# Performance work log

Measured on AMD Instinct MI355X. Metric: run time of the kernel, lower is better.

## Reference

```python
import jax, jax.numpy as jnp
import numpy as np

B, L, D_MODEL = 2, 2048, 1024
EXPAND, D_STATE, D_CONV = 2, 16, 4
D_INNER = EXPAND * D_MODEL          # 2048
DT_RANK = D_MODEL // 16             # 64 (mamba-ssm 'auto' rank)


def setup_inputs() -> dict:
    key = jax.random.key(0)
    ks = jax.random.split(key, 8)
    s = lambda k, shape, scale: jax.random.normal(k, shape, jnp.float32) * scale
    x = s(ks[0], (B, L, D_MODEL), 1.0)
    W_in = s(ks[1], (2 * D_INNER, D_MODEL), D_MODEL ** -0.5)
    conv_w = s(ks[2], (D_INNER, 1, D_CONV), D_CONV ** -0.5)   # depthwise kernel
    conv_b = s(ks[3], (D_INNER,), 0.02)
    W_xproj = s(ks[4], (DT_RANK + 2 * D_STATE, D_INNER), D_INNER ** -0.5)
    W_dt = s(ks[5], (D_INNER, DT_RANK), DT_RANK ** -0.5)
    # inverse-softplus of dt ~= 0.01 (mamba default dt init region)
    b_dt = jnp.log(jnp.expm1(0.01 * jnp.ones((D_INNER,), jnp.float32)))
    # S4D-real init: A = -[1..d_state] per channel
    A_log = jnp.log(jnp.broadcast_to(
        jnp.arange(1, D_STATE + 1, dtype=jnp.float32), (D_INNER, D_STATE)))
    D = jnp.ones((D_INNER,), jnp.float32)
    W_out = s(ks[6], (D_MODEL, D_INNER), D_INNER ** -0.5)
    return dict(x=x, W_in=W_in, conv_w=conv_w, conv_b=conv_b, W_xproj=W_xproj,
                W_dt=W_dt, b_dt=b_dt, A_log=A_log, D=D, W_out=W_out)


def reference(x, W_in, conv_w, conv_b, W_xproj, W_dt, b_dt, A_log, D, W_out):
    # in_proj: [B,L,d_model] -> [B,L,2*d_inner]
    xz = jnp.einsum('bld,ed->ble', x, W_in)
    xs, z = jnp.split(xz, 2, axis=-1)

    # causal depthwise conv1d over time, kernel d_conv
    xc = jnp.swapaxes(xs, 1, 2)  # [B, d_inner, L]
    xc = jax.lax.conv_general_dilated(
        xc, conv_w, window_strides=(1,), padding=[(D_CONV - 1, 0)],
        feature_group_count=D_INNER)
    xc = xc + conv_b[None, :, None]
    xs = jax.nn.silu(jnp.swapaxes(xc, 1, 2))  # [B,L,d_inner]

    # x_proj -> (dt, B, C)
    x_dbl = jnp.einsum('bld,ed->ble', xs, W_xproj)
    dt, Bm, Cm = jnp.split(x_dbl, [DT_RANK, DT_RANK + D_STATE], axis=-1)
    dt = jax.nn.softplus(jnp.einsum('blr,dr->bld', dt, W_dt) + b_dt)  # [B,L,d_inner]

    A = -jnp.exp(A_log)  # [d_inner, d_state]

    def step(h, inp):
        dt_t, B_t, C_t, x_t = inp  # [B,d], [B,n], [B,n], [B,d]
        dA = jnp.exp(dt_t[..., None] * A)                       # [B,d,n]
        h = h * dA + (dt_t * x_t)[..., None] * B_t[:, None, :]  # [B,d,n]
        y = jnp.einsum('bdn,bn->bd', h, C_t)
        return h, y

    tm = lambda a: jnp.swapaxes(a, 0, 1)  # time-major for scan
    h0 = jnp.zeros((x.shape[0], D_INNER, D_STATE), x.dtype)
    _, ys = jax.lax.scan(step, h0, (tm(dt), tm(Bm), tm(Cm), tm(xs)))

    y = tm(ys) + xs * D          # skip term D*x
    y = y * jax.nn.silu(z)       # gate
    return jnp.einsum('bld,ed->ble', y, W_out)  # out_proj -> [B,L,d_model]
```

## Files before the change

kernel.cpp:

```cpp
#include <hip/hip_runtime.h>
#include <cstdint>
#include <cstddef>

typedef __bf16 bf16_t;
typedef bf16_t bf16x4 __attribute__((ext_vector_type(4)));
typedef bf16_t bf16x8 __attribute__((ext_vector_type(8)));
typedef float f32x4 __attribute__((ext_vector_type(4)));

static __device__ __forceinline__ void glds16(const void* g, void* l) {
    __builtin_amdgcn_global_load_lds((const __attribute__((address_space(1))) void*)g,
                                     (__attribute__((address_space(3))) void*)l,
                                     16, 0, 0);
}

#define BARRIER()  asm volatile("s_barrier" ::: "memory")
#define DS_WAIT()  do { asm volatile("s_waitcnt lgkmcnt(0)" ::: "memory"); \
                        __builtin_amdgcn_sched_barrier(0); } while (0)

__global__ __launch_bounds__(256)
void cast5(const float* __restrict__ s0, bf16_t* __restrict__ d0, int n0,
           const float* __restrict__ s1, bf16_t* __restrict__ d1, int n1,
           const float* __restrict__ s2, bf16_t* __restrict__ d2, int n2,
           const float* __restrict__ s3, bf16_t* __restrict__ d3, int n3,
           const float* __restrict__ s4, bf16_t* __restrict__ d4)
{
    int bb = blockIdx.x;
    const float* s; bf16_t* d;
    if (bb < n0)              { s = s0; d = d0; }
    else if ((bb -= n0) < n1) { s = s1; d = d1; }
    else if ((bb -= n1) < n2) { s = s2; d = d2; }
    else if ((bb -= n2) < n3) { s = s3; d = d3; }
    else                      { bb -= n3; s = s4; d = d4; }
    const size_t base = (size_t)bb * 1024 + threadIdx.x * 4;
    const f32x4 v = *(const f32x4*)(s + base);
    bf16x4 o;
    o[0] = (bf16_t)v[0]; o[1] = (bf16_t)v[1]; o[2] = (bf16_t)v[2]; o[3] = (bf16_t)v[3];
    *(bf16x4*)(d + base) = o;
}

#define LOAD_A(MQ) \
    _Pragma("unroll") for (int mf = 0; mf < 4; ++mf) { \
        aF[mf][0] = *(const bf16x8*)(Ab + (aRow + (MQ)*64 + mf*16)*64 + ck0); \
        aF[mf][1] = *(const bf16x8*)(Ab + (aRow + (MQ)*64 + mf*16)*64 + ck1); }

#define LOAD_B(NQ, dst) \
    _Pragma("unroll") for (int nf = 0; nf < 2; ++nf) { \
        dst[nf][0] = *(const bf16x8*)(Bb + (bRow + (NQ)*32 + nf*16)*64 + ck0); \
        dst[nf][1] = *(const bf16x8*)(Bb + (bRow + (NQ)*32 + nf*16)*64 + ck1); }

#define MFMA16(MQ, NQ, bset) \
    __builtin_amdgcn_s_setprio(1); \
    _Pragma("unroll") for (int mf = 0; mf < 4; ++mf) \
    _Pragma("unroll") for (int nf = 0; nf < 2; ++nf) \
    _Pragma("unroll") for (int kk = 0; kk < 2; ++kk) \
        acc[(MQ)*4+mf][(NQ)*2+nf] = __builtin_amdgcn_mfma_f32_16x16x32_bf16( \
            aF[mf][kk], bset[nf][kk], acc[(MQ)*4+mf][(NQ)*2+nf], 0, 0, 0); \
    __builtin_amdgcn_s_setprio(0);

template<int EPI, int SPLITK>
__global__ __launch_bounds__(512, 2)
void gemm256_bt(const bf16_t* __restrict__ A, const bf16_t* __restrict__ Bt,
                const int N, const int K, const int KC,
                bf16_t* __restrict__ o0, bf16_t* __restrict__ o1)
{
    constexpr int TILE = 256 * 64;
    __shared__ __align__(16) bf16_t As[2 * TILE];
    __shared__ __align__(16) bf16_t Bs[2 * TILE];

    const int tid  = threadIdx.x;
    const int lane = tid & 63;
    const int w    = tid >> 6;
    const int wm   = w >> 2, wn = w & 3;
    const int l16  = lane & 15, quad = lane >> 4;
    const int e7   = l16 & 7;
    const int ck0  = (quad ^ e7) << 3;
    const int ck1  = ck0 ^ 32;
    const int lr   = lane >> 3, l8 = lane & 7;
    const int swz  = (l8 ^ lr) << 3;
    const int m0   = blockIdx.y * 256, n0 = blockIdx.x * 256;
    const int NT   = KC >> 6;

    const int aRow = wm * 128 + l16;
    const int bRow = wn * 64 + l16;

    f32x4 acc[8][4] = {};
    bf16x8 aF[4][2], bLo[2][2], bHi[2][2];

    auto STAGE = [&](int unit, int kt, int d) {
        const bf16_t* g; int rg0; bf16_t* lb; int rbase;
        if (unit <= 1) { g = A;  rg0 = m0; lb = As;
                         rbase = unit * 64 + w * 8; }
        else           { g = Bt; rg0 = n0; lb = Bs;
                         rbase = ((w >> 2) << 6) + ((w & 3) << 3) + ((unit & 1) << 5); }
#pragma unroll
        for (int L = 0; L < 2; ++L) {
            const int rb = rbase + L * 128;
            glds16(g + (size_t)(rg0 + rb + lr) * K + kt * 64 + swz,
                   lb + d * TILE + rb * 64);
        }
    };

    STAGE(2, 0, 0); STAGE(0, 0, 0); STAGE(3, 0, 0); STAGE(1, 0, 0);
    if (NT > 1) { STAGE(2, 1, 1); STAGE(0, 1, 1); STAGE(3, 1, 1); }
    if (NT > 1) asm volatile("s_waitcnt vmcnt(6)" ::: "memory");
    else        asm volatile("s_waitcnt vmcnt(0)" ::: "memory");
    BARRIER();

    for (int i = 0; i < NT; ++i) {
        const int b = i & 1;
        const bf16_t* Ab = As + b * TILE;
        const bf16_t* Bb = Bs + b * TILE;

        LOAD_A(0); LOAD_B(0, bLo);
        if (i + 1 < NT) STAGE(1, i + 1, (i + 1) & 1);
        BARRIER(); DS_WAIT();
        MFMA16(0, 0, bLo);
        __builtin_amdgcn_sched_barrier(0);
        BARRIER();

        LOAD_B(1, bHi);
        if (i + 2 < NT) STAGE(2, i + 2, b);
        BARRIER(); DS_WAIT();
        MFMA16(0, 1, bHi);
        __builtin_amdgcn_sched_barrier(0);
        BARRIER();

        LOAD_A(1);
        if (i + 2 < NT) { STAGE(0, i + 2, b); STAGE(3, i + 2, b); }
        BARRIER(); DS_WAIT();
        MFMA16(1, 1, bHi);
        MFMA16(1, 0, bLo);
        __builtin_amdgcn_sched_barrier(0);
        if (i + 2 < NT) asm volatile("s_waitcnt vmcnt(6)" ::: "memory");
        else            asm volatile("s_waitcnt vmcnt(0)" ::: "memory");
        BARRIER();
    }

#pragma unroll
    for (int mf = 0; mf < 8; ++mf)
#pragma unroll
        for (int nf = 0; nf < 4; ++nf)
#pragma unroll
            for (int r = 0; r < 4; ++r) {
                const int gr = m0 + wm * 128 + mf * 16 + quad * 4 + r;
                const int gc = n0 + wn * 64 + nf * 16 + l16;
                const float v = acc[mf][nf][r];
                if (EPI == 1) {
                    if (gc < 2048) o0[(size_t)gr * 2048 + gc] = (bf16_t)v;
                    else           o1[(size_t)gr * 2048 + (gc - 2048)] = (bf16_t)v;
                } else {
                    ((float*)o0)[(size_t)gr * N + gc] = v;
                }
            }
}

template<int EPI>
__global__ __launch_bounds__(256)
void gemm_bt(const bf16_t* __restrict__ A, const bf16_t* __restrict__ Bt,
             const int M, const int N, const int K,
             void* __restrict__ o0, void* __restrict__ o1,
             const float* __restrict__ bias)
{
    __shared__ __align__(16) bf16_t As[128 * 64];
    __shared__ __align__(16) bf16_t Bs[128 * 64];

    const int tid  = threadIdx.x;
    const int lane = tid & 63;
    const int wave = tid >> 6;
    const int wm = wave & 1, wn = wave >> 1;
    const int m0 = blockIdx.y * 128, n0 = blockIdx.x * 128;
    const int quad = lane >> 4, l16 = lane & 15;

    f32x4 acc[4][4] = {};

    for (int k0 = 0; k0 < K; k0 += 64) {
        __syncthreads();
#pragma unroll
        for (int j = 0; j < 4; j++) {
            const int u  = wave * 2048 + j * 512;
            const int ue = u + lane * 8;
            const int row = ue >> 6, col = ue & 63;
            glds16(A  + (size_t)(m0 + row) * K + k0 + col, As + u);
            glds16(Bt + (size_t)(n0 + row) * K + k0 + col, Bs + u);
        }
        __syncthreads();

#pragma unroll
        for (int kk = 0; kk < 2; kk++) {
            bf16x8 afr[4], bfr[4];
#pragma unroll
            for (int mt = 0; mt < 4; mt++)
                afr[mt] = *(const bf16x8*)(As + (wm * 64 + mt * 16 + l16) * 64 + kk * 32 + quad * 8);
#pragma unroll
            for (int nt = 0; nt < 4; nt++)
                bfr[nt] = *(const bf16x8*)(Bs + (wn * 64 + nt * 16 + l16) * 64 + kk * 32 + quad * 8);
#pragma unroll
            for (int mt = 0; mt < 4; mt++)
#pragma unroll
                for (int nt = 0; nt < 4; nt++)
                    acc[mt][nt] = __builtin_amdgcn_mfma_f32_16x16x32_bf16(
                        afr[mt], bfr[nt], acc[mt][nt], 0, 0, 0);
        }
    }

#pragma unroll
    for (int mt = 0; mt < 4; mt++)
#pragma unroll
        for (int nt = 0; nt < 4; nt++)
#pragma unroll
            for (int r = 0; r < 4; r++) {
                const int gr = m0 + wm * 64 + mt * 16 + quad * 4 + r;
                const int gc = n0 + wn * 64 + nt * 16 + l16;
                const float v = acc[mt][nt][r];
                if (EPI == 0) {
                    ((float*)o0)[(size_t)gr * N + gc] = v;
                } else if (EPI == 2) {
                    const float t  = v + bias[gc];
                    const float sp = (t > 15.f) ? t : __logf(1.f + __expf(t));
                    ((bf16_t*)o0)[(size_t)gr * 2048 + gc] = (bf16_t)sp;
                }
            }
}

__global__ __launch_bounds__(256)
void conv_xproj_dt(const bf16_t* __restrict__ xs_pre,
                   const float* __restrict__ cw, const float* __restrict__ cb,
                   const bf16_t* __restrict__ Wxp, const bf16_t* __restrict__ Wdt,
                   const float* __restrict__ bdt,
                   bf16_t* __restrict__ xs, bf16_t* __restrict__ dt,
                   float* __restrict__ Bm, float* __restrict__ Cm)
{
    __shared__ __align__(16) bf16_t xsL[16 * 2048];
    __shared__ float red[4][64][25];
    __shared__ __align__(16) bf16_t dtA[16 * 64];

    const int tid  = threadIdx.x;
    const int lane = tid & 63, w = tid >> 6;
    const int m0   = blockIdx.x * 16;
    const int l16  = lane & 15, quad = lane >> 4, l8 = lane & 7;
    const int l0   = m0 & 2047;

    {
        const int d0 = tid * 8;
        float w0[8], w1[8], w2[8], w3[8], bs[8];
#pragma unroll
        for (int j = 0; j < 8; j++) {
            const f32x4 wv = *(const f32x4*)(cw + (size_t)(d0 + j) * 4);
            w0[j] = wv[0]; w1[j] = wv[1]; w2[j] = wv[2]; w3[j] = wv[3];
            bs[j] = cb[d0 + j];
        }
        const int r1 = (m0 >= 1) ? m0 - 1 : 0;
        const int r2 = (m0 >= 2) ? m0 - 2 : 0;
        const int r3 = (m0 >= 3) ? m0 - 3 : 0;
        const bf16x8 v1 = *(const bf16x8*)(xs_pre + (size_t)r1 * 2048 + d0);
        const bf16x8 v2 = *(const bf16x8*)(xs_pre + (size_t)r2 * 2048 + d0);
        const bf16x8 v3 = *(const bf16x8*)(xs_pre + (size_t)r3 * 2048 + d0);
        float p1[8], p2[8], p3[8];
#pragma unroll
        for (int j = 0; j < 8; j++) {
            p1[j] = (float)v1[j]; p2[j] = (float)v2[j]; p3[j] = (float)v3[j];
        }
#pragma unroll
        for (int r = 0; r < 16; r++) {
            const int l = l0 + r;
            const float m1 = (l >= 1) ? 1.f : 0.f;
            const float m2 = (l >= 2) ? 1.f : 0.f;
            const float m3 = (l >= 3) ? 1.f : 0.f;
            const bf16x8 v = *(const bf16x8*)(xs_pre + (size_t)(m0 + r) * 2048 + d0);
            bf16x8 o;
#pragma unroll
            for (int j = 0; j < 8; j++) {
                const float cur = (float)v[j];
                float a = bs[j] + w3[j] * cur;
                a += m1 * w2[j] * p1[j];
                a += m2 * w1[j] * p2[j];
                a += m3 * w0[j] * p3[j];
                const float s = a / (1.f + __expf(-a));
                o[j] = (bf16_t)s;
                p3[j] = p2[j]; p2[j] = p1[j]; p1[j] = cur;
            }
            *(bf16x8*)(xs + (size_t)(m0 + r) * 2048 + d0) = o;
            const int g = (d0 >> 3) ^ (r & 7);
            *(bf16x8*)(xsL + r * 2048 + g * 8) = o;
        }
    }
    __syncthreads();

    f32x4 acc[6] = {};
    const int kbase = w * 512;
    for (int k0 = 0; k0 < 512; k0 += 32) {
        const int gA = ((kbase + k0) >> 3) + quad;
        const bf16x8 afr = *(const bf16x8*)(xsL + (size_t)l16 * 2048 + ((gA ^ l8) << 3));
#pragma unroll
        for (int t = 0; t < 6; t++) {
            const bf16x8 bfr = *(const bf16x8*)(Wxp + (size_t)(t * 16 + l16) * 2048 + kbase + k0 + quad * 8);
            acc[t] = __builtin_amdgcn_mfma_f32_16x16x32_bf16(afr, bfr, acc[t], 0, 0, 0);
        }
    }
#pragma unroll
    for (int t = 0; t < 6; t++)
#pragma unroll
        for (int r = 0; r < 4; r++) red[w][lane][t * 4 + r] = acc[t][r];
    __syncthreads();

    {
#pragma unroll
        for (int r = 0; r < 4; r++) {
            const int j = w * 4 + r;
            const float v = red[0][lane][j] + red[1][lane][j]
                          + red[2][lane][j] + red[3][lane][j];
            const int row = quad * 4 + r, col = w * 16 + l16;
            const int g = (col >> 3) ^ (row & 7);
            dtA[row * 64 + g * 8 + (col & 7)] = (bf16_t)v;
        }
        if (w == 0) {
#pragma unroll
            for (int t = 4; t < 6; t++)
#pragma unroll
                for (int r = 0; r < 4; r++) {
                    const int j = t * 4 + r;
                    const float v = red[0][lane][j] + red[1][lane][j]
                                  + red[2][lane][j] + red[3][lane][j];
                    const int gr = m0 + quad * 4 + r;
                    const int gc = t * 16 + l16;
                    if (gc < 80) Bm[(size_t)gr * 16 + (gc - 64)] = v;
                    else         Cm[(size_t)gr * 16 + (gc - 80)] = v;
                }
        }
    }
    __syncthreads();

    const bf16x8 a0 = *(const bf16x8*)(dtA + l16 * 64 + (((0 + quad) ^ l8) << 3));
    const bf16x8 a1 = *(const bf16x8*)(dtA + l16 * 64 + (((4 + quad) ^ l8) << 3));
    for (int nt = 0; nt < 32; ++nt) {
        const int nb = w * 512 + nt * 16;
        const bf16x8 b0 = *(const bf16x8*)(Wdt + (size_t)(nb + l16) * 64 + quad * 8);
        const bf16x8 b1 = *(const bf16x8*)(Wdt + (size_t)(nb + l16) * 64 + 32 + quad * 8);
        f32x4 a = {};
        a = __builtin_amdgcn_mfma_f32_16x16x32_bf16(a0, b0, a, 0, 0, 0);
        a = __builtin_amdgcn_mfma_f32_16x16x32_bf16(a1, b1, a, 0, 0, 0);
        const int gc = nb + l16;
        const float bv = bdt[gc];
#pragma unroll
        for (int r = 0; r < 4; r++) {
            const int gr = m0 + quad * 4 + r;
            const float t  = a[r] + bv;
            const float sp = (t > 15.f) ? t : __logf(1.f + __expf(t));
            dt[(size_t)gr * 2048 + gc] = (bf16_t)sp;
        }
    }
}

__global__ __launch_bounds__(256)
void conv_silu(const bf16_t* __restrict__ xs_pre, const float* __restrict__ cw,
               const float* __restrict__ cb, bf16_t* __restrict__ xs)
{
    const int d0 = threadIdx.x * 8;
    const int rg = blockIdx.x * 8;
    float w0[8], w1[8], w2[8], w3[8], bs[8];
#pragma unroll
    for (int j = 0; j < 8; j++) {
        const f32x4 wv = *(const f32x4*)(cw + (size_t)(d0 + j) * 4);
        w0[j] = wv[0]; w1[j] = wv[1]; w2[j] = wv[2]; w3[j] = wv[3];
        bs[j] = cb[d0 + j];
    }
    float p1[8], p2[8], p3[8];
    {
        const int r1 = (rg >= 1) ? rg - 1 : 0;
        const int r2 = (rg >= 2) ? rg - 2 : 0;
        const int r3 = (rg >= 3) ? rg - 3 : 0;
        const bf16x8 v1 = *(const bf16x8*)(xs_pre + (size_t)r1 * 2048 + d0);
        const bf16x8 v2 = *(const bf16x8*)(xs_pre + (size_t)r2 * 2048 + d0);
        const bf16x8 v3 = *(const bf16x8*)(xs_pre + (size_t)r3 * 2048 + d0);
#pragma unroll
        for (int j = 0; j < 8; j++) {
            p1[j] = (float)v1[j]; p2[j] = (float)v2[j]; p3[j] = (float)v3[j];
        }
    }
#pragma unroll
    for (int t = 0; t < 8; t++) {
        const int r = rg + t;
        const int l = r & 2047;
        const float m1 = (l >= 1) ? 1.f : 0.f;
        const float m2 = (l >= 2) ? 1.f : 0.f;
        const float m3 = (l >= 3) ? 1.f : 0.f;
        const bf16x8 v = *(const bf16x8*)(xs_pre + (size_t)r * 2048 + d0);
        bf16x8 o;
#pragma unroll
        for (int j = 0; j < 8; j++) {
            const float cur = (float)v[j];
            float a = bs[j] + w3[j] * cur;
            a += m1 * w2[j] * p1[j];
            a += m2 * w1[j] * p2[j];
            a += m3 * w0[j] * p3[j];
            const float s = a / (1.f + __expf(-a));
            o[j] = (bf16_t)s;
            p3[j] = p2[j]; p2[j] = p1[j]; p1[j] = cur;
        }
        *(bf16x8*)(xs + (size_t)r * 2048 + d0) = o;
    }
}

__global__ __launch_bounds__(256)
void xproj_kernel(const bf16_t* __restrict__ A, const bf16_t* __restrict__ Bt,
                  bf16_t* __restrict__ dtr, float* __restrict__ Bm, float* __restrict__ Cm)
{
    __shared__ float red[4][64][25];
    const int tid  = threadIdx.x;
    const int lane = tid & 63, w = tid >> 6;
    const int m0 = blockIdx.x * 16;
    const int l16 = lane & 15, quad = lane >> 4;
    f32x4 acc[6] = {};

    const int kbase = w * 512;
    const bf16_t* ap = A + (size_t)(m0 + l16) * 2048 + kbase + quad * 8;
    for (int k0 = 0; k0 < 512; k0 += 32) {
        const bf16x8 afr = *(const bf16x8*)(ap + k0);
#pragma unroll
        for (int t = 0; t < 6; t++) {
            const bf16x8 bfr = *(const bf16x8*)(Bt + (size_t)(t * 16 + l16) * 2048 + kbase + k0 + quad * 8);
            acc[t] = __builtin_amdgcn_mfma_f32_16x16x32_bf16(afr, bfr, acc[t], 0, 0, 0);
        }
    }
#pragma unroll
    for (int t = 0; t < 6; t++)
#pragma unroll
        for (int r = 0; r < 4; r++) red[w][lane][t * 4 + r] = acc[t][r];
    __syncthreads();
    if (w == 0) {
#pragma unroll
        for (int t = 0; t < 6; t++)
#pragma unroll
            for (int r = 0; r < 4; r++) {
                const int j = t * 4 + r;
                const float v = red[0][lane][j] + red[1][lane][j]
                              + red[2][lane][j] + red[3][lane][j];
                const int gr = m0 + quad * 4 + r;
                const int gc = t * 16 + l16;
                if (gc < 64)      dtr[(size_t)gr * 64 + gc] = (bf16_t)v;
                else if (gc < 80) Bm[(size_t)gr * 16 + (gc - 64)] = v;
                else              Cm[(size_t)gr * 16 + (gc - 80)] = v;
            }
    }
}

static __device__ __forceinline__ bool fast_check(const float* A_log, int d, float& a1) {
    a1 = -__expf(A_log[(size_t)d * 16]);
    bool ok = true;
#pragma unroll
    for (int n = 1; n < 16; n++) {
        const float an = -__expf(A_log[(size_t)d * 16 + n]);
        const float pn = (float)(n + 1) * a1;
        ok = ok && (fabsf(an - pn) <= 1e-3f * fabsf(pn) + 1e-6f);
    }
    return ok;
}

__global__ __launch_bounds__(256)
void scan1(const bf16_t* __restrict__ dt, const bf16_t* __restrict__ xs,
           const float* __restrict__ Bm, const float* __restrict__ A_log,
           float* __restrict__ sdt_o, bf16_t* __restrict__ Hsum)
{
    const int tid = threadIdx.x;
    const int bi  = blockIdx.x;
    const int c   = bi & 63;
    const int bb  = bi >> 6;
    const int b   = bb >> 3;
    const int d   = (bb & 7) * 256 + tid;
    float a1; const bool fast = fast_check(A_log, d, a1);

    float h[16] = {};
    float s = 0.f;
    const size_t rowbase = (size_t)b * 2048 + c * 32;

    if (fast) {
#pragma unroll 4
        for (int t = 0; t < 32; t++) {
            const size_t ro = (rowbase + t) * 2048 + d;
            const float dtv = (float)dt[ro];
            const float xv  = (float)xs[ro];
            s += dtv;
            const float r = __expf(dtv * a1);
            float rp[16]; rp[0] = r;
#pragma unroll
            for (int n = 1; n < 16; n++) rp[n] = rp[n - 1] * r;
            const float bx = dtv * xv;
            const float* bp = Bm + (rowbase + t) * 16;
#pragma unroll
            for (int n = 0; n < 16; n++) h[n] = fmaf(h[n], rp[n], bx * bp[n]);
        }
    } else {
        for (int t = 0; t < 32; t++) {
            const size_t ro = (rowbase + t) * 2048 + d;
            const float dtv = (float)dt[ro];
            const float xv  = (float)xs[ro];
            s += dtv;
            const float bx = dtv * xv;
            const float* bp = Bm + (rowbase + t) * 16;
#pragma unroll
            for (int n = 0; n < 16; n++) {
                const float an = -__expf(A_log[(size_t)d * 16 + n]);
                h[n] = fmaf(h[n], __expf(dtv * an), bx * bp[n]);
            }
        }
    }
    const size_t sb = (size_t)bi * 256 + tid;
    sdt_o[sb] = s;
    bf16x8 h0, h1;
#pragma unroll
    for (int n = 0; n < 8; n++) { h0[n] = (bf16_t)h[n]; h1[n] = (bf16_t)h[n + 8]; }
    *(bf16x8*)(Hsum + sb * 16)     = h0;
    *(bf16x8*)(Hsum + sb * 16 + 8) = h1;
}

__global__ __launch_bounds__(256)
void scan2(const float* __restrict__ sdt, bf16_t* __restrict__ Hsum,
           const float* __restrict__ A_log)
{
    const int tid = threadIdx.x;
    const int bb  = blockIdx.x;
    const int d   = (bb & 7) * 256 + tid;
    float a1; const bool fast = fast_check(A_log, d, a1);

    float h[16] = {};
    if (fast) {
        size_t sb = (size_t)(bb * 64) * 256 + tid;
        float sA = sdt[sb];
        bf16x8 hA0 = *(const bf16x8*)(Hsum + sb * 16);
        bf16x8 hA1 = *(const bf16x8*)(Hsum + sb * 16 + 8);
        float sB = 0.f; bf16x8 hB0 = {}, hB1 = {};
        {
            const size_t sb1 = sb + 256;
            sB  = sdt[sb1];
            hB0 = *(const bf16x8*)(Hsum + sb1 * 16);
            hB1 = *(const bf16x8*)(Hsum + sb1 * 16 + 8);
        }
        for (int c = 0; c < 64; c++) {
            float sC = 0.f; bf16x8 hC0 = {}, hC1 = {};
            if (c + 2 < 64) {
                const size_t sb2 = sb + 512;
                sC  = sdt[sb2];
                hC0 = *(const bf16x8*)(Hsum + sb2 * 16);
                hC1 = *(const bf16x8*)(Hsum + sb2 * 16 + 8);
            }
            bf16x8 o0, o1;
#pragma unroll
            for (int n = 0; n < 8; n++) { o0[n] = (bf16_t)h[n]; o1[n] = (bf16_t)h[n + 8]; }
            *(bf16x8*)(Hsum + sb * 16)     = o0;
            *(bf16x8*)(Hsum + sb * 16 + 8) = o1;
            const float r = __expf(sA * a1);
            float rp[16]; rp[0] = r;
#pragma unroll
            for (int n = 1; n < 16; n++) rp[n] = rp[n - 1] * r;
#pragma unroll
            for (int n = 0; n < 16; n++) {
                const float hsv = (n < 8) ? (float)hA0[n] : (float)hA1[n - 8];
                h[n] = fmaf(h[n], rp[n], hsv);
            }
            sb += 256;
            sA = sB; hA0 = hB0; hA1 = hB1;
            sB = sC; hB0 = hC0; hB1 = hC1;
        }
    } else {
        for (int c = 0; c < 64; c++) {
            const size_t sb = ((size_t)(bb * 64 + c) * 256 + tid);
            const float s = sdt[sb];
            bf16x8 hs0 = *(const bf16x8*)(Hsum + sb * 16);
            bf16x8 hs1 = *(const bf16x8*)(Hsum + sb * 16 + 8);
            bf16x8 o0, o1;
#pragma unroll
            for (int n = 0; n < 8; n++) { o0[n] = (bf16_t)h[n]; o1[n] = (bf16_t)h[n + 8]; }
            *(bf16x8*)(Hsum + sb * 16)     = o0;
            *(bf16x8*)(Hsum + sb * 16 + 8) = o1;
#pragma unroll
            for (int n = 0; n < 16; n++) {
                const float an = -__expf(A_log[(size_t)d * 16 + n]);
                const float hsv = (n < 8) ? (float)hs0[n] : (float)hs1[n - 8];
                h[n] = fmaf(h[n], __expf(s * an), hsv);
            }
        }
    }
}

__global__ __launch_bounds__(256)
void scan3(const bf16_t* __restrict__ dt, const bf16_t* __restrict__ xs,
           bf16_t* __restrict__ zy,
           const float* __restrict__ Bm, const float* __restrict__ Cm,
           const float* __restrict__ A_log, const float* __restrict__ Dv,
           const bf16_t* __restrict__ Hseed)
{
    const int tid = threadIdx.x;
    const int bi  = blockIdx.x;
    const int c   = bi & 63;
    const int bb  = bi >> 6;
    const int b   = bb >> 3;
    const int d   = (bb & 7) * 256 + tid;
    float a1; const bool fast = fast_check(A_log, d, a1);
    const float Dd = Dv[d];

    const size_t sb = (size_t)bi * 256 + tid;
    const bf16x8 hs0 = *(const bf16x8*)(Hseed + sb * 16);
    const bf16x8 hs1 = *(const bf16x8*)(Hseed + sb * 16 + 8);
    float h[16];
#pragma unroll
    for (int n = 0; n < 8; n++) { h[n] = (float)hs0[n]; h[n + 8] = (float)hs1[n]; }

    const size_t rowbase = (size_t)b * 2048 + c * 32;

    if (fast) {
#pragma unroll 2
        for (int t = 0; t < 32; t++) {
            const size_t ro = (rowbase + t) * 2048 + d;
            const float dtv = (float)dt[ro];
            const float xv  = (float)xs[ro];
            const float zv  = (float)zy[ro];
            const float r = __expf(dtv * a1);
            float rp[16]; rp[0] = r;
#pragma unroll
            for (int n = 1; n < 16; n++) rp[n] = rp[n - 1] * r;
            const float bx = dtv * xv;
            const float* bp = Bm + (rowbase + t) * 16;
            const float* cp = Cm + (rowbase + t) * 16;
            float y0 = 0.f, y1 = 0.f;
#pragma unroll
            for (int n = 0; n < 16; n += 2) {
                h[n]     = fmaf(h[n],     rp[n],     bx * bp[n]);
                h[n + 1] = fmaf(h[n + 1], rp[n + 1], bx * bp[n + 1]);
                y0 = fmaf(h[n],     cp[n],     y0);
                y1 = fmaf(h[n + 1], cp[n + 1], y1);
            }
            const float yv = (y0 + y1) + xv * Dd;
            const float g  = zv / (1.f + __expf(-zv));
            zy[ro] = (bf16_t)(yv * g);
        }
    } else {
        for (int t = 0; t < 32; t++) {
            const size_t ro = (rowbase + t) * 2048 + d;
            const float dtv = (float)dt[ro];
            const float xv  = (float)xs[ro];
            const float zv  = (float)zy[ro];
            const float bx = dtv * xv;
            const float* bp = Bm + (rowbase + t) * 16;
            const float* cp = Cm + (rowbase + t) * 16;
            float y = 0.f;
#pragma unroll
            for (int n = 0; n < 16; n++) {
                const float an = -__expf(A_log[(size_t)d * 16 + n]);
                h[n] = fmaf(h[n], __expf(dtv * an), bx * bp[n]);
                y = fmaf(h[n], cp[n], y);
            }
            const float yv = y + xv * Dd;
            const float g  = zv / (1.f + __expf(-zv));
            zy[ro] = (bf16_t)(yv * g);
        }
    }
}

extern "C" void kernel_launch(void* const* d_in, const int* in_sizes, int n_in,
                              void* d_out, int out_size, void* d_ws, size_t ws_size,
                              hipStream_t stream)
{
    const float* x     = (const float*)d_in[0];
    const float* W_in  = (const float*)d_in[1];
    const float* convw = (const float*)d_in[2];
    const float* convb = (const float*)d_in[3];
    const float* W_xp  = (const float*)d_in[4];
    const float* W_dt  = (const float*)d_in[5];
    const float* b_dt  = (const float*)d_in[6];
    const float* A_log = (const float*)d_in[7];
    const float* Dv    = (const float*)d_in[8];
    const float* W_out = (const float*)d_in[9];

    char* ws = (char*)d_ws;
    bf16_t* bufP   = (bf16_t*)(ws + 0);
    bf16_t* bufZ   = (bf16_t*)(ws + 16777216);
    bf16_t* bufX   = (bf16_t*)(ws + 33554432);
    bf16_t* W_in_b = (bf16_t*)(ws + 33554432);
    bf16_t* dtr    = (bf16_t*)(ws + 50331648);
    float*  Bm     = (float*)(ws + 50855936);
    float*  Cm     = (float*)(ws + 51118080);
    float*  sdt    = (float*)(ws + 51380224);
    bf16_t* Hsum   = (bf16_t*)(ws + 52428800);
    bf16_t* x_b    = (bf16_t*)(ws + 52428800);
    bf16_t* W_out_b= (bf16_t*)(ws + 60817408);
    bf16_t* W_xp_b = (bf16_t*)(ws + 65011712);
    bf16_t* W_dt_b = (bf16_t*)(ws + 65404928);
    bf16_t* dtb    = (bf16_t*)(ws + 65667072);
    const bool fuse = (ws_size >= 82444288ull);

    cast5<<<dim3(4096 + 4096 + 2048 + 192 + 128), dim3(256), 0, stream>>>(
        x, x_b, 4096, W_in, W_in_b, 4096, W_out, W_out_b, 2048,
        W_xp, W_xp_b, 192, W_dt, W_dt_b);

    gemm256_bt<1, 1><<<dim3(16, 16), dim3(512), 0, stream>>>(
        x_b, W_in_b, 4096, 1024, 1024, bufP, bufZ);

    bf16_t* dtp = fuse ? dtb : bufP;
    if (fuse) {
        conv_xproj_dt<<<dim3(256), dim3(256), 0, stream>>>(
            bufP, convw, convb, W_xp_b, W_dt_b, b_dt, bufX, dtb, Bm, Cm);
    } else {
        conv_silu<<<dim3(512), dim3(256), 0, stream>>>(bufP, convw, convb, bufX);
        xproj_kernel<<<dim3(256), dim3(256), 0, stream>>>(bufX, W_xp_b, dtr, Bm, Cm);
        gemm_bt<2><<<dim3(16, 32), dim3(256), 0, stream>>>(
            dtr, W_dt_b, 4096, 2048, 64, (void*)bufP, nullptr, b_dt);
    }

    scan1<<<dim3(1024), dim3(256), 0, stream>>>(dtp, bufX, Bm, A_log, sdt, Hsum);
    scan2<<<dim3(16),   dim3(256), 0, stream>>>(sdt, Hsum, A_log);
    scan3<<<dim3(1024), dim3(256), 0, stream>>>(dtp, bufX, bufZ, Bm, Cm, A_log, Dv, Hsum);

    gemm_bt<0><<<dim3(8, 32), dim3(256), 0, stream>>>(
        bufZ, W_out_b, 4096, 1024, 2048, d_out, nullptr, nullptr);
}
```

Measured before the change: 280.8 us.

## Store xs and dt channel-major for scans; split-K the output projection

The conv and dt-projection kernels now write xs and dt transposed as [d_inner, B*L], so each scan thread can read its 32 time steps as contiguous bf16x8 vectors instead of one scalar per step with a 2048-element stride. The output GEMM is split along K into two halves that accumulate with atomic adds into an output zeroed by a memset, which doubles the block count. The costs are an extra memset, atomic traffic, and strided scalar loads in the non-fused xproj path. The z gate in scan3 is still read row-major.

```diff
diff --git a/kernel.cpp b/kernel.cpp
--- a/kernel.cpp
+++ b/kernel.cpp
@@ -154,7 +154,7 @@
             }
 }
 
-template<int EPI>
+template<int EPI, int SPLITK>
 __global__ __launch_bounds__(256)
 void gemm_bt(const bf16_t* __restrict__ A, const bf16_t* __restrict__ Bt,
              const int M, const int N, const int K,
@@ -170,10 +170,13 @@
     const int wm = wave & 1, wn = wave >> 1;
     const int m0 = blockIdx.y * 128, n0 = blockIdx.x * 128;
     const int quad = lane >> 4, l16 = lane & 15;
+    const int z   = (SPLITK > 1) ? blockIdx.z : 0;
+    const int KC  = K / SPLITK;
+    const int kb  = z * KC;
 
     f32x4 acc[4][4] = {};
 
-    for (int k0 = 0; k0 < K; k0 += 64) {
+    for (int k0 = kb; k0 < kb + KC; k0 += 64) {
         __syncthreads();
 #pragma unroll
         for (int j = 0; j < 4; j++) {
@@ -212,12 +215,14 @@
                 const int gr = m0 + wm * 64 + mt * 16 + quad * 4 + r;
                 const int gc = n0 + wn * 64 + nt * 16 + l16;
                 const float v = acc[mt][nt][r];
-                if (EPI == 0) {
-                    ((float*)o0)[(size_t)gr * N + gc] = v;
+                if (EPI == 4) {
+                    unsafeAtomicAdd((float*)o0 + (size_t)gr * N + gc, v);
                 } else if (EPI == 2) {
                     const float t  = v + bias[gc];
                     const float sp = (t > 15.f) ? t : __logf(1.f + __expf(t));
-                    ((bf16_t*)o0)[(size_t)gr * 2048 + gc] = (bf16_t)sp;
+                    ((bf16_t*)o0)[(size_t)gc * 4096 + gr] = (bf16_t)sp;
+                } else {
+                    ((float*)o0)[(size_t)gr * N + gc] = v;
                 }
             }
 }
@@ -227,7 +232,7 @@
                    const float* __restrict__ cw, const float* __restrict__ cb,
                    const bf16_t* __restrict__ Wxp, const bf16_t* __restrict__ Wdt,
                    const float* __restrict__ bdt,
-                   bf16_t* __restrict__ xs, bf16_t* __restrict__ dt,
+                   bf16_t* __restrict__ xsT, bf16_t* __restrict__ dtT,
                    float* __restrict__ Bm, float* __restrict__ Cm)
 {
     __shared__ __align__(16) bf16_t xsL[16 * 2048];
@@ -260,6 +265,7 @@
         for (int j = 0; j < 8; j++) {
             p1[j] = (float)v1[j]; p2[j] = (float)v2[j]; p3[j] = (float)v3[j];
         }
+        bf16x8 o_keep[16];
 #pragma unroll
         for (int r = 0; r < 16; r++) {
             const int l = l0 + r;
@@ -279,9 +285,17 @@
                 o[j] = (bf16_t)s;
                 p3[j] = p2[j]; p2[j] = p1[j]; p1[j] = cur;
             }
-            *(bf16x8*)(xs + (size_t)(m0 + r) * 2048 + d0) = o;
+            o_keep[r] = o;
             const int g = (d0 >> 3) ^ (r & 7);
             *(bf16x8*)(xsL + r * 2048 + g * 8) = o;
+        }
+#pragma unroll
+        for (int j = 0; j < 8; j++) {
+            bf16x8 lo, hi;
+#pragma unroll
+            for (int rr = 0; rr < 8; rr++) { lo[rr] = o_keep[rr][j]; hi[rr] = o_keep[rr + 8][j]; }
+            *(bf16x8*)(xsT + (size_t)(d0 + j) * 4096 + m0)     = lo;
+            *(bf16x8*)(xsT + (size_t)(d0 + j) * 4096 + m0 + 8) = hi;
         }
     }
     __syncthreads();
@@ -332,6 +346,7 @@
 
     const bf16x8 a0 = *(const bf16x8*)(dtA + l16 * 64 + (((0 + quad) ^ l8) << 3));
     const bf16x8 a1 = *(const bf16x8*)(dtA + l16 * 64 + (((4 + quad) ^ l8) << 3));
+    const int gr0 = m0 + quad * 4;
     for (int nt = 0; nt < 32; ++nt) {
         const int nb = w * 512 + nt * 16;
         const bf16x8 b0 = *(const bf16x8*)(Wdt + (size_t)(nb + l16) * 64 + quad * 8);
@@ -341,19 +356,20 @@
         a = __builtin_amdgcn_mfma_f32_16x16x32_bf16(a1, b1, a, 0, 0, 0);
         const int gc = nb + l16;
         const float bv = bdt[gc];
+        bf16x4 dw;
 #pragma unroll
         for (int r = 0; r < 4; r++) {
-            const int gr = m0 + quad * 4 + r;
             const float t  = a[r] + bv;
             const float sp = (t > 15.f) ? t : __logf(1.f + __expf(t));
-            dt[(size_t)gr * 2048 + gc] = (bf16_t)sp;
-        }
+            dw[r] = (bf16_t)sp;
+        }
+        *(bf16x4*)(dtT + (size_t)gc * 4096 + gr0) = dw;
     }
 }
 
 __global__ __launch_bounds__(256)
 void conv_silu(const bf16_t* __restrict__ xs_pre, const float* __restrict__ cw,
-               const float* __restrict__ cb, bf16_t* __restrict__ xs)
+               const float* __restrict__ cb, bf16_t* __restrict__ xsT)
 {
     const int d0 = threadIdx.x * 8;
     const int rg = blockIdx.x * 8;
@@ -377,6 +393,7 @@
             p1[j] = (float)v1[j]; p2[j] = (float)v2[j]; p3[j] = (float)v3[j];
         }
     }
+    bf16x8 o_keep[8];
 #pragma unroll
     for (int t = 0; t < 8; t++) {
         const int r = rg + t;
@@ -397,12 +414,19 @@
             o[j] = (bf16_t)s;
             p3[j] = p2[j]; p2[j] = p1[j]; p1[j] = cur;
         }
-        *(bf16x8*)(xs + (size_t)r * 2048 + d0) = o;
+        o_keep[t] = o;
+    }
+#pragma unroll
+    for (int j = 0; j < 8; j++) {
+        bf16x8 col;
+#pragma unroll
+        for (int tt = 0; tt < 8; tt++) col[tt] = o_keep[tt][j];
+        *(bf16x8*)(xsT + (size_t)(d0 + j) * 4096 + rg) = col;
     }
 }
 
 __global__ __launch_bounds__(256)
-void xproj_kernel(const bf16_t* __restrict__ A, const bf16_t* __restrict__ Bt,
+void xproj_kernel(const bf16_t* __restrict__ xsT, const bf16_t* __restrict__ Bt,
                   bf16_t* __restrict__ dtr, float* __restrict__ Bm, float* __restrict__ Cm)
 {
     __shared__ float red[4][64][25];
@@ -413,9 +437,11 @@
     f32x4 acc[6] = {};
 
     const int kbase = w * 512;
-    const bf16_t* ap = A + (size_t)(m0 + l16) * 2048 + kbase + quad * 8;
     for (int k0 = 0; k0 < 512; k0 += 32) {
-        const bf16x8 afr = *(const bf16x8*)(ap + k0);
+        bf16x8 afr;
+#pragma unroll
+        for (int e = 0; e < 8; e++)
+            afr[e] = xsT[(size_t)(kbase + k0 + quad * 8 + e) * 4096 + m0 + l16];
 #pragma unroll
         for (int t = 0; t < 6; t++) {
             const bf16x8 bfr = *(const bf16x8*)(Bt + (size_t)(t * 16 + l16) * 2048 + kbase + k0 + quad * 8);
@@ -457,7 +483,7 @@
 }
 
 __global__ __launch_bounds__(256)
-void scan1(const bf16_t* __restrict__ dt, const bf16_t* __restrict__ xs,
+void scan1(const bf16_t* __restrict__ dtT, const bf16_t* __restrict__ xsT,
            const float* __restrict__ Bm, const float* __restrict__ A_log,
            float* __restrict__ sdt_o, bf16_t* __restrict__ Hsum)
 {
@@ -472,30 +498,39 @@
     float h[16] = {};
     float s = 0.f;
     const size_t rowbase = (size_t)b * 2048 + c * 32;
+    const bf16_t* dp = dtT + (size_t)d * 4096 + rowbase;
+    const bf16_t* xp = xsT + (size_t)d * 4096 + rowbase;
 
     if (fast) {
-#pragma unroll 4
-        for (int t = 0; t < 32; t++) {
-            const size_t ro = (rowbase + t) * 2048 + d;
-            const float dtv = (float)dt[ro];
-            const float xv  = (float)xs[ro];
-            s += dtv;
-            const float r = __expf(dtv * a1);
-            float rp[16]; rp[0] = r;
-#pragma unroll
-            for (int n = 1; n < 16; n++) rp[n] = rp[n - 1] * r;
-            const float bx = dtv * xv;
-            const float* bp = Bm + (rowbase + t) * 16;
-#pragma unroll
-            for (int n = 0; n < 16; n++) h[n] = fmaf(h[n], rp[n], bx * bp[n]);
-        }
+        bf16x8 dv[4], xv[4];
+#pragma unroll
+        for (int q = 0; q < 4; q++) {
+            dv[q] = *(const bf16x8*)(dp + q * 8);
+            xv[q] = *(const bf16x8*)(xp + q * 8);
+        }
+#pragma unroll
+        for (int q = 0; q < 4; q++)
+#pragma unroll
+            for (int tt = 0; tt < 8; tt++) {
+                const int t = q * 8 + tt;
+                const float dtv = (float)dv[q][tt];
+                const float xvv = (float)xv[q][tt];
+                s += dtv;
+                const float r = __expf(dtv * a1);
+                float rp[16]; rp[0] = r;
+#pragma unroll
+                for (int n = 1; n < 16; n++) rp[n] = rp[n - 1] * r;
+                const float bx = dtv * xvv;
+                const float* bp = Bm + (rowbase + t) * 16;
+#pragma unroll
+                for (int n = 0; n < 16; n++) h[n] = fmaf(h[n], rp[n], bx * bp[n]);
+            }
     } else {
         for (int t = 0; t < 32; t++) {
-            const size_t ro = (rowbase + t) * 2048 + d;
-            const float dtv = (float)dt[ro];
-            const float xv  = (float)xs[ro];
+            const float dtv = (float)dp[t];
+            const float xvv = (float)xp[t];
             s += dtv;
-            const float bx = dtv * xv;
+            const float bx = dtv * xvv;
             const float* bp = Bm + (rowbase + t) * 16;
 #pragma unroll
             for (int n = 0; n < 16; n++) {
@@ -583,7 +618,7 @@
 }
 
 __global__ __launch_bounds__(256)
-void scan3(const bf16_t* __restrict__ dt, const bf16_t* __restrict__ xs,
+void scan3(const bf16_t* __restrict__ dtT, const bf16_t* __restrict__ xsT,
            bf16_t* __restrict__ zy,
            const float* __restrict__ Bm, const float* __restrict__ Cm,
            const float* __restrict__ A_log, const float* __restrict__ Dv,
@@ -606,40 +641,51 @@
     for (int n = 0; n < 8; n++) { h[n] = (float)hs0[n]; h[n + 8] = (float)hs1[n]; }
 
     const size_t rowbase = (size_t)b * 2048 + c * 32;
+    const bf16_t* dp = dtT + (size_t)d * 4096 + rowbase;
+    const bf16_t* xp = xsT + (size_t)d * 4096 + rowbase;
 
     if (fast) {
-#pragma unroll 2
-        for (int t = 0; t < 32; t++) {
-            const size_t ro = (rowbase + t) * 2048 + d;
-            const float dtv = (float)dt[ro];
-            const float xv  = (float)xs[ro];
-            const float zv  = (float)zy[ro];
-            const float r = __expf(dtv * a1);
-            float rp[16]; rp[0] = r;
-#pragma unroll
-            for (int n = 1; n < 16; n++) rp[n] = rp[n - 1] * r;
-            const float bx = dtv * xv;
-            const float* bp = Bm + (rowbase + t) * 16;
-            const float* cp = Cm + (rowbase + t) * 16;
-            float y0 = 0.f, y1 = 0.f;
-#pragma unroll
-            for (int n = 0; n < 16; n += 2) {
-                h[n]     = fmaf(h[n],     rp[n],     bx * bp[n]);
-                h[n + 1] = fmaf(h[n + 1], rp[n + 1], bx * bp[n + 1]);
-                y0 = fmaf(h[n],     cp[n],     y0);
-                y1 = fmaf(h[n + 1], cp[n + 1], y1);
-            }
-            const float yv = (y0 + y1) + xv * Dd;
-            const float g  = zv / (1.f + __expf(-zv));
-            zy[ro] = (bf16_t)(yv * g);
-        }
+        bf16x8 dv[4], xv[4];
+#pragma unroll
+        for (int q = 0; q < 4; q++) {
+            dv[q] = *(const bf16x8*)(dp + q * 8);
+            xv[q] = *(const bf16x8*)(xp + q * 8);
+        }
+#pragma unroll
+        for (int q = 0; q < 4; q++)
+#pragma unroll
+            for (int tt = 0; tt < 8; tt++) {
+                const int t = q * 8 + tt;
+                const size_t ro = (rowbase + t) * 2048 + d;
+                const float dtv = (float)dv[q][tt];
+                const float xvv = (float)xv[q][tt];
+                const float zv  = (float)zy[ro];
+                const float r = __expf(dtv * a1);
+                float rp[16]; rp[0] = r;
+#pragma unroll
+                for (int n = 1; n < 16; n++) rp[n] = rp[n - 1] * r;
+                const float bx = dtv * xvv;
+                const float* bp = Bm + (rowbase + t) * 16;
+                const float* cp = Cm + (rowbase + t) * 16;
+                float y0 = 0.f, y1 = 0.f;
+#pragma unroll
+                for (int n = 0; n < 16; n += 2) {
+                    h[n]     = fmaf(h[n],     rp[n],     bx * bp[n]);
+                    h[n + 1] = fmaf(h[n + 1], rp[n + 1], bx * bp[n + 1]);
+                    y0 = fmaf(h[n],     cp[n],     y0);
+                    y1 = fmaf(h[n + 1], cp[n + 1], y1);
+                }
+                const float yv = (y0 + y1) + xvv * Dd;
+                const float g  = zv / (1.f + __expf(-zv));
+                zy[ro] = (bf16_t)(yv * g);
+            }
     } else {
         for (int t = 0; t < 32; t++) {
             const size_t ro = (rowbase + t) * 2048 + d;
-            const float dtv = (float)dt[ro];
-            const float xv  = (float)xs[ro];
+            const float dtv = (float)dp[t];
+            const float xvv = (float)xp[t];
             const float zv  = (float)zy[ro];
-            const float bx = dtv * xv;
+            const float bx = dtv * xvv;
             const float* bp = Bm + (rowbase + t) * 16;
             const float* cp = Cm + (rowbase + t) * 16;
             float y = 0.f;
@@ -649,7 +695,7 @@
                 h[n] = fmaf(h[n], __expf(dtv * an), bx * bp[n]);
                 y = fmaf(h[n], cp[n], y);
             }
-            const float yv = y + xv * Dd;
+            const float yv = y + xvv * Dd;
             const float g  = zv / (1.f + __expf(-zv));
             zy[ro] = (bf16_t)(yv * g);
         }
@@ -691,6 +737,7 @@
     cast5<<<dim3(4096 + 4096 + 2048 + 192 + 128), dim3(256), 0, stream>>>(
         x, x_b, 4096, W_in, W_in_b, 4096, W_out, W_out_b, 2048,
         W_xp, W_xp_b, 192, W_dt, W_dt_b);
+    hipMemsetAsync(d_out, 0, (size_t)out_size, stream);
 
     gemm256_bt<1, 1><<<dim3(16, 16), dim3(512), 0, stream>>>(
         x_b, W_in_b, 4096, 1024, 1024, bufP, bufZ);
@@ -702,7 +749,7 @@
     } else {
         conv_silu<<<dim3(512), dim3(256), 0, stream>>>(bufP, convw, convb, bufX);
         xproj_kernel<<<dim3(256), dim3(256), 0, stream>>>(bufX, W_xp_b, dtr, Bm, Cm);
-        gemm_bt<2><<<dim3(16, 32), dim3(256), 0, stream>>>(
+        gemm_bt<2, 1><<<dim3(16, 32), dim3(256), 0, stream>>>(
             dtr, W_dt_b, 4096, 2048, 64, (void*)bufP, nullptr, b_dt);
     }
 
@@ -710,6 +757,6 @@
     scan2<<<dim3(16),   dim3(256), 0, stream>>>(sdt, Hsum, A_log);
     scan3<<<dim3(1024), dim3(256), 0, stream>>>(dtp, bufX, bufZ, Bm, Cm, A_log, Dv, Hsum);
 
-    gemm_bt<0><<<dim3(8, 32), dim3(256), 0, stream>>>(
+    gemm_bt<4, 2><<<dim3(8, 32, 2), dim3(256), 0, stream>>>(
         bufZ, W_out_b, 4096, 1024, 2048, d_out, nullptr, nullptr);
 }
```

Result: slower. 321.8 us (+14.6%).
